# Optimization experiments

Hardware: AMD Instinct MI355X
Metric: run time of the kernel (lower is better)

## Reference

```python
import jax, jax.numpy as jnp
import numpy as np

N_NODES = 50000
N_EDGES = 800000
D_IN = 96
D_OUT = 96


def setup_inputs() -> dict:
    key = jax.random.key(0)
    k1, k2, k3, k4, k5, k6 = jax.random.split(key, 6)
    x = jax.random.normal(k1, (N_NODES, D_IN), dtype=jnp.float32)
    edge_index = jax.random.randint(k2, (2, N_EDGES), 0, N_NODES, dtype=jnp.int32)
    W_lin = jax.random.normal(k3, (D_OUT, D_IN), dtype=jnp.float32) * 0.1
    b_lin = jax.random.normal(k4, (D_OUT,), dtype=jnp.float32) * 0.1
    W_root = jax.random.normal(k5, (D_OUT, D_IN), dtype=jnp.float32) * 0.1
    b_root = jax.random.normal(k6, (D_OUT,), dtype=jnp.float32) * 0.1
    return {"x": x, "edge_index": edge_index, "W_lin": W_lin, "b_lin": b_lin,
            "W_root": W_root, "b_root": b_root}


def reference(x, edge_index, W_lin, b_lin, W_root, b_root):
    # GCNConv with separate root weight: out = relu(scatter_add(norm * lin(x_src), dst) + root(x))
    src, dst = edge_index[0], edge_index[1]
    n = x.shape[0]
    # symmetric degree normalization (in-degree based, clamped to avoid div0)
    deg = jax.ops.segment_sum(jnp.ones(src.shape[0], dtype=x.dtype), dst, num_segments=n)
    dinv = jax.lax.rsqrt(jnp.maximum(deg, 1.0))
    norm = dinv[src] * dinv[dst]                      # [E]
    h = x @ W_lin.T + b_lin                           # [N, D_OUT] neighbor transform
    msgs = h[src] * norm[:, None]                     # [E, D_OUT] gathered + scaled
    agg = jax.ops.segment_sum(msgs, dst, num_segments=n)  # scatter-add
    out = agg + x @ W_root.T + b_root                 # root/self contribution
    return jax.nn.relu(out)
```

## Files before the change

### kernel.cpp

```cpp
#include <hip/hip_runtime.h>

#define D 96
#define BSH 5
#define NBMAX 1600
#define BCAP 832
#define SCAP 1088
#define CH 8192

typedef __attribute__((ext_vector_type(8))) short bf16x8;
typedef __attribute__((ext_vector_type(4))) float f32x4;

__device__ __forceinline__ unsigned bf16_rne(float f) {
    unsigned u = __float_as_uint(f);
    return (u + 0x7fffu + ((u >> 16) & 1u)) >> 16;
}
__device__ __forceinline__ float blo(unsigned u) { return __uint_as_float(u << 16); }
__device__ __forceinline__ float bhi(unsigned u) { return __uint_as_float(u & 0xffff0000u); }

__global__ __launch_bounds__(512) void binh_kernel(
    const int* __restrict__ ei, int* __restrict__ bcur, unsigned* __restrict__ bp,
    const float* __restrict__ Wlin, const float* __restrict__ Wroot,
    unsigned* __restrict__ wfrag, int E, int NB)
{
    __shared__ int hist[NBMAX];
    __shared__ int lstart[NBMAX];
    __shared__ int gbase[NBMAX];
    __shared__ unsigned stage[CH];
    int t = threadIdx.x;
    int gt = blockIdx.x * 512 + t;
    int e0 = blockIdx.x * CH;
    int ne = min(CH, E - e0);
    for (int i = t; i < NB; i += 512) hist[i] = 0;
    if (gt < 9216) {
        int f = gt >> 8, r = gt & 255;
        int l = r >> 2, jp = r & 3;
        int ct = f / 6, st = f % 6;
        int nn = ct * 16 + (l & 15);
        int k  = st * 32 + (l >> 4) * 8 + jp * 2;
        const float* W = (k < D) ? Wlin : Wroot;
        int kk = (k < D) ? k : k - D;
        float v0 = W[nn * D + kk], v1 = W[nn * D + kk + 1];
        wfrag[gt] = bf16_rne(v0) | (bf16_rne(v1) << 16);
    }
    __syncthreads();
    unsigned pk[16]; int bk[16];
    int base = e0 + t * 16;
    #pragma unroll
    for (int q = 0; q < 4; ++q) {
        int b4 = base + q * 4;
        if (b4 + 3 < E) {
            int4 a = *(const int4*)(ei + b4);
            int4 b = *(const int4*)(ei + E + b4);
            pk[q*4+0] = (unsigned)a.x | ((unsigned)b.x << 16); bk[q*4+0] = b.x >> BSH;
            pk[q*4+1] = (unsigned)a.y | ((unsigned)b.y << 16); bk[q*4+1] = b.y >> BSH;
            pk[q*4+2] = (unsigned)a.z | ((unsigned)b.z << 16); bk[q*4+2] = b.z >> BSH;
            pk[q*4+3] = (unsigned)a.w | ((unsigned)b.w << 16); bk[q*4+3] = b.w >> BSH;
        } else {
            #pragma unroll
            for (int u = 0; u < 4; ++u) {
                int e = b4 + u;
                if (e < E) { pk[q*4+u] = (unsigned)ei[e] | ((unsigned)ei[E + e] << 16); bk[q*4+u] = ei[E + e] >> BSH; }
                else bk[q*4+u] = -1;
            }
        }
    }
    #pragma unroll
    for (int u = 0; u < 16; ++u)
        if (bk[u] >= 0) atomicAdd(&hist[bk[u]], 1);
    __syncthreads();
    if (t < 64) {
        int lane = t, carry = 0;
        for (int c0 = 0; c0 < NB; c0 += 64) {
            int i = c0 + lane;
            int v = (i < NB) ? hist[i] : 0;
            int incl = v;
            #pragma unroll
            for (int d = 1; d < 64; d <<= 1) {
                int uu = __shfl_up(incl, d, 64);
                if (lane >= d) incl += uu;
            }
            if (i < NB) lstart[i] = carry + incl - v;
            carry += __shfl(incl, 63, 64);
        }
    }
    __syncthreads();
    for (int i = t; i < NB; i += 512) {
        int c = hist[i];
        if (c > 0) gbase[i] = atomicAdd(&bcur[i], c);
        hist[i] = lstart[i];
    }
    __syncthreads();
    #pragma unroll
    for (int u = 0; u < 16; ++u) {
        if (bk[u] >= 0) {
            int p = atomicAdd(&hist[bk[u]], 1);
            stage[p] = pk[u];
        }
    }
    __syncthreads();
    for (int i = t; i < ne; i += 512) {
        unsigned w = stage[i];
        int b = (int)(w >> (16 + BSH));
        int slot = gbase[b] + (i - lstart[b]);
        if (slot < BCAP) bp[(size_t)b * BCAP + slot] = w;
    }
}

__global__ __launch_bounds__(256) void prep_kernel(
    const int* __restrict__ bcur, const unsigned* __restrict__ bp,
    const float* __restrict__ x, float* __restrict__ dinv,
    unsigned* __restrict__ xs, int n)
{
    __shared__ int hist[32];
    int t = threadIdx.x;
    int node0 = blockIdx.x << BSH;
    int ne = min(bcur[blockIdx.x], BCAP);
    const unsigned* bpb = bp + (size_t)blockIdx.x * BCAP;
    if (blockIdx.x == 0) {
        if (t < 48) xs[(size_t)n * 48 + t] = 0u;
        if (t == 48) dinv[n] = 0.f;
    }
    if (t < 32) hist[t] = 0;
    __syncthreads();
    for (int i = t; i < ne; i += 256) atomicAdd(&hist[(bpb[i] >> 16) & 31], 1);
    __syncthreads();
    for (int task = t; task < 32 * 24; task += 256) {
        int row = task / 24, q = task - row * 24;
        int node = node0 + row;
        if (node < n) {
            int d = hist[row];
            float dr = rsqrtf((float)(d > 1 ? d : 1));
            float4 v = ((const float4*)x)[(size_t)node * 24 + q];
            uint2 o;
            o.x = bf16_rne(dr * v.x) | (bf16_rne(dr * v.y) << 16);
            o.y = bf16_rne(dr * v.z) | (bf16_rne(dr * v.w) << 16);
            *(uint2*)(xs + (size_t)node * 48 + q * 2) = o;
            if (q == 0) dinv[node] = dr;
        }
    }
}

__global__ __launch_bounds__(512) void bgather_gemm_kernel(
    const int* __restrict__ bcur, const unsigned* __restrict__ bp,
    const float* __restrict__ dinv, const unsigned* __restrict__ xs,
    const unsigned* __restrict__ wfrag, const float* __restrict__ blin,
    const float* __restrict__ broot, float* __restrict__ out, int n)
{
    __shared__ unsigned ssrc[SCAP];
    __shared__ int hist[32];
    __shared__ int seg[33];
    __shared__ int cur[32];
    __shared__ unsigned yt[32][52];
    __shared__ float sv32[32];
    int t = threadIdx.x;
    int node0 = blockIdx.x << BSH;
    int ne = min(bcur[blockIdx.x], BCAP);
    const unsigned* bpb = bp + (size_t)blockIdx.x * BCAP;
    const unsigned ZR = (unsigned)n;
    if (t < 32) hist[t] = 0;
    if (t >= 32 && t < 40) ssrc[t - 32] = ZR;
    __syncthreads();
    unsigned wreg[2]; int cnt = 0;
    for (int i = t; i < ne; i += 512) {
        wreg[cnt] = bpb[i];
        atomicAdd(&hist[(wreg[cnt] >> 16) & 31], 1);
        ++cnt;
    }
    __syncthreads();
    if (t == 0) {
        int run = 8;
        #pragma unroll
        for (int i = 0; i < 32; ++i) { seg[i] = run; run += (hist[i] + 7) & ~7; }
        seg[32] = run;
    }
    __syncthreads();
    if (t < 32) cur[t] = seg[t];
    __syncthreads();
    cnt = 0;
    for (int i = t; i < ne; i += 512) {
        int p = atomicAdd(&cur[(wreg[cnt] >> 16) & 31], 1);
        ssrc[p] = wreg[cnt] & 0xffffu;
        ++cnt;
    }
    __syncthreads();
    if (t < 32) {
        for (int p = seg[t] + hist[t]; p < seg[t + 1]; ++p) ssrc[p] = ZR;
    }
    __syncthreads();

    int wv = t >> 6, l = t & 63;
    for (int p = wv * 4; p < wv * 4 + 4; p += 2) {
        int ndA = p, ndB = p + 1;
        int jsA = seg[ndA], itA = (seg[ndA + 1] - jsA) >> 3;
        int jsB = seg[ndB], itB = (seg[ndB + 1] - jsB) >> 3;
        int iters = itA > itB ? itA : itB;
        float a0A = 0.f, a1A = 0.f, a0B = 0.f, a1B = 0.f, sn = 0.f;
        for (int it = 0; it < iters; ++it) {
            int baseA = (it < itA) ? (jsA + it * 8) : 0;
            int baseB = (it < itB) ? (jsB + it * 8) : 0;
            uint4 iA0 = *(const uint4*)(&ssrc[baseA]);
            uint4 iA1 = *(const uint4*)(&ssrc[baseA + 4]);
            uint4 iB0 = *(const uint4*)(&ssrc[baseB]);
            uint4 iB1 = *(const uint4*)(&ssrc[baseB + 4]);
            unsigned suA[8] = {iA0.x, iA0.y, iA0.z, iA0.w, iA1.x, iA1.y, iA1.z, iA1.w};
            unsigned suB[8] = {iB0.x, iB0.y, iB0.z, iB0.w, iB1.x, iB1.y, iB1.z, iB1.w};
            if (l < 48) {
                unsigned uvA[8], uvB[8];
                #pragma unroll
                for (int u = 0; u < 8; ++u) uvA[u] = xs[(size_t)suA[u] * 48 + l];
                #pragma unroll
                for (int u = 0; u < 8; ++u) uvB[u] = xs[(size_t)suB[u] * 48 + l];
                #pragma unroll
                for (int u = 0; u < 8; ++u) { a0A += blo(uvA[u]); a1A += bhi(uvA[u]); }
                #pragma unroll
                for (int u = 0; u < 8; ++u) { a0B += blo(uvB[u]); a1B += bhi(uvB[u]); }
            } else if (l < 56) {
                sn += dinv[suA[l - 48]];
            } else {
                sn += dinv[suB[l - 56]];
            }
        }
        float stA = 0.f, stB = 0.f;
        #pragma unroll
        for (int u = 0; u < 8; ++u) {
            stA += __shfl(sn, 48 + u, 64);
            stB += __shfl(sn, 56 + u, 64);
        }
        int nodeA = node0 + ndA, nodeB = node0 + ndB;
        float dnA = (nodeA < n) ? dinv[nodeA] : 0.f;
        float dnB = (nodeB < n) ? dinv[nodeB] : 0.f;
        if (l < 48) {
            yt[ndA][l] = bf16_rne(dnA * a0A) | (bf16_rne(dnA * a1A) << 16);
            yt[ndB][l] = bf16_rne(dnB * a0B) | (bf16_rne(dnB * a1B) << 16);
        } else if (l == 48) {
            sv32[ndA] = dnA * stA;
            sv32[ndB] = dnB * stB;
        }
    }
    __syncthreads();

    int lane15 = l & 15, quad = l >> 4;
    for (int j = wv; j < 12; j += 8) {
        int rg = j / 6, ct = j % 6;
        int r0 = node0 + rg * 16;
        f32x4 accY = (f32x4){0.f, 0.f, 0.f, 0.f};
        f32x4 accX = (f32x4){0.f, 0.f, 0.f, 0.f};
        #pragma unroll
        for (int st_ = 0; st_ < 3; ++st_) {
            bf16x8 a = *(const bf16x8*)(&yt[rg * 16 + lane15][st_ * 16 + quad * 4]);
            bf16x8 b = *(const bf16x8*)(wfrag + ((ct * 6 + st_) * 64 + l) * 4);
            accY = __builtin_amdgcn_mfma_f32_16x16x32_bf16(a, b, accY, 0, 0, 0);
        }
        int ar = r0 + lane15;
        #pragma unroll
        for (int sm = 0; sm < 3; ++sm) {
            bf16x8 a = (bf16x8){0, 0, 0, 0, 0, 0, 0, 0};
            if (ar < n) a = *(const bf16x8*)(xs + (size_t)ar * 48 + sm * 16 + quad * 4);
            bf16x8 b = *(const bf16x8*)(wfrag + ((ct * 6 + 3 + sm) * 64 + l) * 4);
            accX = __builtin_amdgcn_mfma_f32_16x16x32_bf16(a, b, accX, 0, 0, 0);
        }
        int col = ct * 16 + lane15;
        float blc = blin[col], brc = broot[col];
        #pragma unroll
        for (int reg = 0; reg < 4; ++reg) {
            int r = r0 + quad * 4 + reg;
            if (r < n) {
                float sv = sv32[rg * 16 + quad * 4 + reg];
                float rd = 1.0f / dinv[r];
                float v = accY[reg] + rd * accX[reg] + sv * blc + brc;
                out[(size_t)r * D + col] = fmaxf(v, 0.f);
            }
        }
    }
}

extern "C" void kernel_launch(void* const* d_in, const int* in_sizes, int n_in,
                              void* d_out, int out_size, void* d_ws, size_t ws_size,
                              hipStream_t stream) {
    const float* x     = (const float*)d_in[0];
    const int*   ei    = (const int*)d_in[1];
    const float* Wlin  = (const float*)d_in[2];
    const float* blin  = (const float*)d_in[3];
    const float* Wroot = (const float*)d_in[4];
    const float* broot = (const float*)d_in[5];
    float* out = (float*)d_out;

    const int n = in_sizes[0] / D;
    const int E = in_sizes[1] / 2;
    const int NB = (n + 31) >> BSH;

    int*      bcur  = (int*)d_ws;
    float*    dinv  = (float*)(bcur + 1600);
    unsigned* bp    = (unsigned*)(dinv + n + 4);
    unsigned* wfrag = bp + (size_t)NB * BCAP;
    unsigned* xs    = wfrag + 9216;

    hipMemsetAsync(bcur, 0, 1600 * sizeof(int), stream);

    binh_kernel<<<(E + CH - 1) / CH, 512, 0, stream>>>(ei, bcur, bp,
                                                       Wlin, Wroot, wfrag, E, NB);
    prep_kernel<<<NB, 256, 0, stream>>>(bcur, bp, x, dinv, xs, n);
    bgather_gemm_kernel<<<NB, 512, 0, stream>>>(bcur, bp, dinv, xs, wfrag,
                                                blin, broot, out, n);
}
```

Before: 146.7 us.

## Fold x bf16 conversion into binning kernel, slim dinv pass, dynamic gather scheduling

The x-to-bf16 conversion moves out of the per-bucket prep kernel into the edge-binning kernel, and xs is no longer prescaled by dinv. dinv is now applied per edge in the gather, and the 1/dinv root rescale is removed. The binning chunk is halved to launch more blocks, with a parallel multi-wave prefix scan. The gather splits each row across two half-waves issuing 8-byte loads, pulls node pairs from a shared-memory work queue, and gets a launch-bounds occupancy hint. This trades a separate bandwidth-bound prep pass and a division for extra per-edge multiplies and shuffle reductions, and the binning kernel now also carries the x conversion work.

```diff
diff --git a/kernel.cpp b/kernel.cpp
--- a/kernel.cpp
+++ b/kernel.cpp
@@ -5,7 +5,7 @@
 #define NBMAX 1600
 #define BCAP 832
 #define SCAP 1088
-#define CH 8192
+#define CH 4096
 
 typedef __attribute__((ext_vector_type(8))) short bf16x8;
 typedef __attribute__((ext_vector_type(4))) float f32x4;
@@ -20,11 +20,13 @@
 __global__ __launch_bounds__(512) void binh_kernel(
     const int* __restrict__ ei, int* __restrict__ bcur, unsigned* __restrict__ bp,
     const float* __restrict__ Wlin, const float* __restrict__ Wroot,
-    unsigned* __restrict__ wfrag, int E, int NB)
+    unsigned* __restrict__ wfrag, const float* __restrict__ x,
+    unsigned* __restrict__ xs, int E, int NB, int n)
 {
     __shared__ int hist[NBMAX];
     __shared__ int lstart[NBMAX];
     __shared__ int gbase[NBMAX];
+    __shared__ int wsum[8];
     __shared__ unsigned stage[CH];
     int t = threadIdx.x;
     int gt = blockIdx.x * 512 + t;
@@ -43,10 +45,10 @@
         wfrag[gt] = bf16_rne(v0) | (bf16_rne(v1) << 16);
     }
     __syncthreads();
-    unsigned pk[16]; int bk[16];
-    int base = e0 + t * 16;
+    unsigned pk[8]; int bk[8];
+    int base = e0 + t * 8;
     #pragma unroll
-    for (int q = 0; q < 4; ++q) {
+    for (int q = 0; q < 2; ++q) {
         int b4 = base + q * 4;
         if (b4 + 3 < E) {
             int4 a = *(const int4*)(ei + b4);
@@ -65,24 +67,36 @@
         }
     }
     #pragma unroll
-    for (int u = 0; u < 16; ++u)
+    for (int u = 0; u < 8; ++u)
         if (bk[u] >= 0) atomicAdd(&hist[bk[u]], 1);
     __syncthreads();
-    if (t < 64) {
-        int lane = t, carry = 0;
-        for (int c0 = 0; c0 < NB; c0 += 64) {
-            int i = c0 + lane;
+    {
+        int wv = t >> 6, l = t & 63;
+        int c0 = wv << 8;
+        int carry = 0;
+        #pragma unroll
+        for (int s = 0; s < 4; ++s) {
+            int i = c0 + (s << 6) + l;
             int v = (i < NB) ? hist[i] : 0;
             int incl = v;
             #pragma unroll
             for (int d = 1; d < 64; d <<= 1) {
                 int uu = __shfl_up(incl, d, 64);
-                if (lane >= d) incl += uu;
+                if (l >= d) incl += uu;
             }
             if (i < NB) lstart[i] = carry + incl - v;
             carry += __shfl(incl, 63, 64);
         }
-    }
+        if (l == 0) wsum[wv] = carry;
+    }
+    __syncthreads();
+    if (t == 0) {
+        int run = 0;
+        #pragma unroll
+        for (int w = 0; w < 8; ++w) { int s = wsum[w]; wsum[w] = run; run += s; }
+    }
+    __syncthreads();
+    for (int i = t; i < NB; i += 512) lstart[i] += wsum[i >> 8];
     __syncthreads();
     for (int i = t; i < NB; i += 512) {
         int c = hist[i];
@@ -91,7 +105,7 @@
     }
     __syncthreads();
     #pragma unroll
-    for (int u = 0; u < 16; ++u) {
+    for (int u = 0; u < 8; ++u) {
         if (bk[u] >= 0) {
             int p = atomicAdd(&hist[bk[u]], 1);
             stage[p] = pk[u];
@@ -104,43 +118,43 @@
         int slot = gbase[b] + (i - lstart[b]);
         if (slot < BCAP) bp[(size_t)b * BCAP + slot] = w;
     }
-}
-
-__global__ __launch_bounds__(256) void prep_kernel(
+    int gsz = gridDim.x * 512;
+    int ntask = (n + 1) * 24;
+    for (int i = gt; i < ntask; i += gsz) {
+        int row = i / 24, q = i - row * 24;
+        uint2 o;
+        if (row < n) {
+            float4 v = ((const float4*)x)[(size_t)row * 24 + q];
+            o.x = bf16_rne(v.x) | (bf16_rne(v.y) << 16);
+            o.y = bf16_rne(v.z) | (bf16_rne(v.w) << 16);
+        } else { o.x = 0u; o.y = 0u; }
+        *(uint2*)(xs + (size_t)row * 48 + q * 2) = o;
+    }
+}
+
+__global__ __launch_bounds__(128) void dinv_kernel(
     const int* __restrict__ bcur, const unsigned* __restrict__ bp,
-    const float* __restrict__ x, float* __restrict__ dinv,
-    unsigned* __restrict__ xs, int n)
+    float* __restrict__ dinv, int n)
 {
     __shared__ int hist[32];
     int t = threadIdx.x;
-    int node0 = blockIdx.x << BSH;
+    if (t < 32) hist[t] = 0;
+    __syncthreads();
     int ne = min(bcur[blockIdx.x], BCAP);
     const unsigned* bpb = bp + (size_t)blockIdx.x * BCAP;
-    if (blockIdx.x == 0) {
-        if (t < 48) xs[(size_t)n * 48 + t] = 0u;
-        if (t == 48) dinv[n] = 0.f;
-    }
-    if (t < 32) hist[t] = 0;
-    __syncthreads();
-    for (int i = t; i < ne; i += 256) atomicAdd(&hist[(bpb[i] >> 16) & 31], 1);
-    __syncthreads();
-    for (int task = t; task < 32 * 24; task += 256) {
-        int row = task / 24, q = task - row * 24;
-        int node = node0 + row;
+    for (int i = t; i < ne; i += 128) atomicAdd(&hist[(bpb[i] >> 16) & 31], 1);
+    __syncthreads();
+    if (t < 32) {
+        int node = (blockIdx.x << BSH) + t;
         if (node < n) {
-            int d = hist[row];
-            float dr = rsqrtf((float)(d > 1 ? d : 1));
-            float4 v = ((const float4*)x)[(size_t)node * 24 + q];
-            uint2 o;
-            o.x = bf16_rne(dr * v.x) | (bf16_rne(dr * v.y) << 16);
-            o.y = bf16_rne(dr * v.z) | (bf16_rne(dr * v.w) << 16);
-            *(uint2*)(xs + (size_t)node * 48 + q * 2) = o;
-            if (q == 0) dinv[node] = dr;
-        }
-    }
-}
-
-__global__ __launch_bounds__(512) void bgather_gemm_kernel(
+            int d = hist[t];
+            dinv[node] = rsqrtf((float)(d > 1 ? d : 1));
+        }
+    }
+    if (blockIdx.x == 0 && t == 32) dinv[n] = 0.f;
+}
+
+__global__ __launch_bounds__(512, 4) void bgather_gemm_kernel(
     const int* __restrict__ bcur, const unsigned* __restrict__ bp,
     const float* __restrict__ dinv, const unsigned* __restrict__ xs,
     const unsigned* __restrict__ wfrag, const float* __restrict__ blin,
@@ -150,6 +164,7 @@
     __shared__ int hist[32];
     __shared__ int seg[33];
     __shared__ int cur[32];
+    __shared__ int pq;
     __shared__ unsigned yt[32][52];
     __shared__ float sv32[32];
     int t = threadIdx.x;
@@ -172,6 +187,7 @@
         #pragma unroll
         for (int i = 0; i < 32; ++i) { seg[i] = run; run += (hist[i] + 7) & ~7; }
         seg[32] = run;
+        pq = 0;
     }
     __syncthreads();
     if (t < 32) cur[t] = seg[t];
@@ -188,36 +204,61 @@
     }
     __syncthreads();
 
-    int wv = t >> 6, l = t & 63;
-    for (int p = wv * 4; p < wv * 4 + 4; p += 2) {
-        int ndA = p, ndB = p + 1;
+    int l = t & 63;
+    int ph = (l >= 24 && l < 48) ? 1 : 0;
+    int m  = l - ph * 24;
+    unsigned loff = (unsigned)(m << 3);
+    const char* xb = (const char*)xs;
+
+    for (;;) {
+        int p;
+        if (l == 0) p = atomicAdd(&pq, 1);
+        p = __shfl(p, 0, 64);
+        if (p >= 16) break;
+        int ndA = p * 2, ndB = ndA + 1;
         int jsA = seg[ndA], itA = (seg[ndA + 1] - jsA) >> 3;
         int jsB = seg[ndB], itB = (seg[ndB + 1] - jsB) >> 3;
         int iters = itA > itB ? itA : itB;
-        float a0A = 0.f, a1A = 0.f, a0B = 0.f, a1B = 0.f, sn = 0.f;
+        float aA0 = 0.f, aA1 = 0.f, aA2 = 0.f, aA3 = 0.f;
+        float aB0 = 0.f, aB1 = 0.f, aB2 = 0.f, aB3 = 0.f;
+        float sn = 0.f;
         for (int it = 0; it < iters; ++it) {
             int baseA = (it < itA) ? (jsA + it * 8) : 0;
             int baseB = (it < itB) ? (jsB + it * 8) : 0;
-            uint4 iA0 = *(const uint4*)(&ssrc[baseA]);
-            uint4 iA1 = *(const uint4*)(&ssrc[baseA + 4]);
-            uint4 iB0 = *(const uint4*)(&ssrc[baseB]);
-            uint4 iB1 = *(const uint4*)(&ssrc[baseB + 4]);
-            unsigned suA[8] = {iA0.x, iA0.y, iA0.z, iA0.w, iA1.x, iA1.y, iA1.z, iA1.w};
-            unsigned suB[8] = {iB0.x, iB0.y, iB0.z, iB0.w, iB1.x, iB1.y, iB1.z, iB1.w};
+            float dvl = 0.f;
+            if (l >= 48) {
+                int bs = (l < 56) ? baseA : baseB;
+                dvl = dinv[ssrc[bs + (l & 7)]];
+                sn += dvl;
+            }
+            uint2 vA0, vA1, vA2, vA3, vB0, vB1, vB2, vB3;
             if (l < 48) {
-                unsigned uvA[8], uvB[8];
-                #pragma unroll
-                for (int u = 0; u < 8; ++u) uvA[u] = xs[(size_t)suA[u] * 48 + l];
-                #pragma unroll
-                for (int u = 0; u < 8; ++u) uvB[u] = xs[(size_t)suB[u] * 48 + l];
-                #pragma unroll
-                for (int u = 0; u < 8; ++u) { a0A += blo(uvA[u]); a1A += bhi(uvA[u]); }
-                #pragma unroll
-                for (int u = 0; u < 8; ++u) { a0B += blo(uvB[u]); a1B += bhi(uvB[u]); }
-            } else if (l < 56) {
-                sn += dinv[suA[l - 48]];
-            } else {
-                sn += dinv[suB[l - 56]];
+                unsigned iA0 = ssrc[baseA + ph],     iA1 = ssrc[baseA + 2 + ph];
+                unsigned iA2 = ssrc[baseA + 4 + ph], iA3 = ssrc[baseA + 6 + ph];
+                unsigned iB0 = ssrc[baseB + ph],     iB1 = ssrc[baseB + 2 + ph];
+                unsigned iB2 = ssrc[baseB + 4 + ph], iB3 = ssrc[baseB + 6 + ph];
+                vA0 = *(const uint2*)(xb + iA0 * 192u + loff);
+                vA1 = *(const uint2*)(xb + iA1 * 192u + loff);
+                vA2 = *(const uint2*)(xb + iA2 * 192u + loff);
+                vA3 = *(const uint2*)(xb + iA3 * 192u + loff);
+                vB0 = *(const uint2*)(xb + iB0 * 192u + loff);
+                vB1 = *(const uint2*)(xb + iB1 * 192u + loff);
+                vB2 = *(const uint2*)(xb + iB2 * 192u + loff);
+                vB3 = *(const uint2*)(xb + iB3 * 192u + loff);
+            }
+            float dA0 = __shfl(dvl, 48 + ph, 64), dA1 = __shfl(dvl, 50 + ph, 64);
+            float dA2 = __shfl(dvl, 52 + ph, 64), dA3 = __shfl(dvl, 54 + ph, 64);
+            float dB0 = __shfl(dvl, 56 + ph, 64), dB1 = __shfl(dvl, 58 + ph, 64);
+            float dB2 = __shfl(dvl, 60 + ph, 64), dB3 = __shfl(dvl, 62 + ph, 64);
+            if (l < 48) {
+                aA0 += dA0 * blo(vA0.x); aA1 += dA0 * bhi(vA0.x); aA2 += dA0 * blo(vA0.y); aA3 += dA0 * bhi(vA0.y);
+                aA0 += dA1 * blo(vA1.x); aA1 += dA1 * bhi(vA1.x); aA2 += dA1 * blo(vA1.y); aA3 += dA1 * bhi(vA1.y);
+                aA0 += dA2 * blo(vA2.x); aA1 += dA2 * bhi(vA2.x); aA2 += dA2 * blo(vA2.y); aA3 += dA2 * bhi(vA2.y);
+                aA0 += dA3 * blo(vA3.x); aA1 += dA3 * bhi(vA3.x); aA2 += dA3 * blo(vA3.y); aA3 += dA3 * bhi(vA3.y);
+                aB0 += dB0 * blo(vB0.x); aB1 += dB0 * bhi(vB0.x); aB2 += dB0 * blo(vB0.y); aB3 += dB0 * bhi(vB0.y);
+                aB0 += dB1 * blo(vB1.x); aB1 += dB1 * bhi(vB1.x); aB2 += dB1 * blo(vB1.y); aB3 += dB1 * bhi(vB1.y);
+                aB0 += dB2 * blo(vB2.x); aB1 += dB2 * bhi(vB2.x); aB2 += dB2 * blo(vB2.y); aB3 += dB2 * bhi(vB2.y);
+                aB0 += dB3 * blo(vB3.x); aB1 += dB3 * bhi(vB3.x); aB2 += dB3 * blo(vB3.y); aB3 += dB3 * bhi(vB3.y);
             }
         }
         float stA = 0.f, stB = 0.f;
@@ -226,12 +267,21 @@
             stA += __shfl(sn, 48 + u, 64);
             stB += __shfl(sn, 56 + u, 64);
         }
+        aA0 += __shfl(aA0, l + 24, 64); aA1 += __shfl(aA1, l + 24, 64);
+        aA2 += __shfl(aA2, l + 24, 64); aA3 += __shfl(aA3, l + 24, 64);
+        aB0 += __shfl(aB0, l + 24, 64); aB1 += __shfl(aB1, l + 24, 64);
+        aB2 += __shfl(aB2, l + 24, 64); aB3 += __shfl(aB3, l + 24, 64);
         int nodeA = node0 + ndA, nodeB = node0 + ndB;
         float dnA = (nodeA < n) ? dinv[nodeA] : 0.f;
         float dnB = (nodeB < n) ? dinv[nodeB] : 0.f;
-        if (l < 48) {
-            yt[ndA][l] = bf16_rne(dnA * a0A) | (bf16_rne(dnA * a1A) << 16);
-            yt[ndB][l] = bf16_rne(dnB * a0B) | (bf16_rne(dnB * a1B) << 16);
+        if (l < 24) {
+            uint2 oA, oB;
+            oA.x = bf16_rne(dnA * aA0) | (bf16_rne(dnA * aA1) << 16);
+            oA.y = bf16_rne(dnA * aA2) | (bf16_rne(dnA * aA3) << 16);
+            oB.x = bf16_rne(dnB * aB0) | (bf16_rne(dnB * aB1) << 16);
+            oB.y = bf16_rne(dnB * aB2) | (bf16_rne(dnB * aB3) << 16);
+            *(uint2*)&yt[ndA][2 * m] = oA;
+            *(uint2*)&yt[ndB][2 * m] = oB;
         } else if (l == 48) {
             sv32[ndA] = dnA * stA;
             sv32[ndB] = dnB * stB;
@@ -239,6 +289,7 @@
     }
     __syncthreads();
 
+    int wv = t >> 6;
     int lane15 = l & 15, quad = l >> 4;
     for (int j = wv; j < 12; j += 8) {
         int rg = j / 6, ct = j % 6;
@@ -266,8 +317,7 @@
             int r = r0 + quad * 4 + reg;
             if (r < n) {
                 float sv = sv32[rg * 16 + quad * 4 + reg];
-                float rd = 1.0f / dinv[r];
-                float v = accY[reg] + rd * accX[reg] + sv * blc + brc;
+                float v = accY[reg] + accX[reg] + sv * blc + brc;
                 out[(size_t)r * D + col] = fmaxf(v, 0.f);
             }
         }
@@ -297,9 +347,9 @@
 
     hipMemsetAsync(bcur, 0, 1600 * sizeof(int), stream);
 
-    binh_kernel<<<(E + CH - 1) / CH, 512, 0, stream>>>(ei, bcur, bp,
-                                                       Wlin, Wroot, wfrag, E, NB);
-    prep_kernel<<<NB, 256, 0, stream>>>(bcur, bp, x, dinv, xs, n);
+    binh_kernel<<<(E + CH - 1) / CH, 512, 0, stream>>>(ei, bcur, bp, Wlin, Wroot,
+                                                       wfrag, x, xs, E, NB, n);
+    dinv_kernel<<<NB, 128, 0, stream>>>(bcur, bp, dinv, n);
     bgather_gemm_kernel<<<NB, 512, 0, stream>>>(bcur, bp, dinv, xs, wfrag,
                                                 blin, broot, out, n);
 }
```

Measured after the change: 147.0 us. About the same (+0.2%).
